# Performance work log

Hardware: AMD Instinct MI355X
Metric: run time of the kernel (lower is better)

## Reference

```python
import jax, jax.numpy as jnp
import numpy as np

B, C, H, W = 2, 512, 64, 64
S = 2            # scale_factor
HEADS = 8
GROUPS = 32      # assumed GroupNorm groups for group_norm(in_channels)
DK = C // HEADS
SCALE = 1.0 / DK ** 2   # faithful to source: 1/d_k**2
RES = H // S
R = RES * 2 - 1


def setup_inputs() -> dict:
    key = jax.random.key(0)
    ks = jax.random.split(key, 8)
    f = lambda k, shp, s=0.02: jax.random.normal(k, shp, jnp.float32) * s
    return {
        "x": jax.random.normal(ks[0], (B, C, H, W), jnp.float32),
        "q_w": f(ks[1], (C, C, 1, 1)),
        "q_b": jnp.zeros((C,), jnp.float32),
        "kv_w": f(ks[2], (2 * C, C, 1, 1)),
        "kv_b": jnp.zeros((2 * C,), jnp.float32),
        "off1_w": f(ks[3], (C, C, S, S)),
        "off1_b": jnp.zeros((C,), jnp.float32),
        "gn_w": jnp.ones((C,), jnp.float32),
        "gn_b": jnp.zeros((C,), jnp.float32),
        "off2_w": f(ks[4], (2, C, 1, 1)),
        "rpe_table": f(ks[5], (HEADS, R, R), 0.01),
        "proj_w": f(ks[6], (C, C, 1, 1)),
        "proj_b": jnp.zeros((C,), jnp.float32),
    }


def _conv(x, w, b=None, stride=1):
    y = jax.lax.conv_general_dilated(x, w, (stride, stride), 'VALID',
                                     dimension_numbers=('NCHW', 'OIHW', 'NCHW'))
    return y if b is None else y + b[None, :, None, None]


def _group_norm(x, w, b, eps=1e-5):
    n, c, h, wd = x.shape
    xg = x.reshape(n, GROUPS, -1)
    mu = xg.mean(-1, keepdims=True)
    var = xg.var(-1, keepdims=True)
    xg = (xg - mu) * jax.lax.rsqrt(var + eps)
    return xg.reshape(n, c, h, wd) * w[None, :, None, None] + b[None, :, None, None]


def _grid_sample(img, grid):
    # bilinear, align_corners=True; img [B,C,H,W], grid [B,...,2] in (x,y) order
    Bn, Cn, Hn, Wn = img.shape
    gshape = grid.shape[1:-1]
    g = grid.reshape(Bn, -1, 2)
    x = (g[..., 0] + 1.0) * 0.5 * (Wn - 1)
    y = (g[..., 1] + 1.0) * 0.5 * (Hn - 1)
    x0 = jnp.floor(x); y0 = jnp.floor(y)
    wx = (x - x0)[:, None, :]; wy = (y - y0)[:, None, :]
    x0i = jnp.clip(x0.astype(jnp.int32), 0, Wn - 1)
    x1i = jnp.clip(x0i + 1, 0, Wn - 1)
    y0i = jnp.clip(y0.astype(jnp.int32), 0, Hn - 1)
    y1i = jnp.clip(y0i + 1, 0, Hn - 1)
    imf = img.reshape(Bn, Cn, Hn * Wn)
    gat = lambda yi, xi: jnp.take_along_axis(imf, (yi * Wn + xi)[:, None, :], axis=2)
    out = (gat(y0i, x0i) * (1 - wx) * (1 - wy) + gat(y0i, x1i) * wx * (1 - wy)
           + gat(y1i, x0i) * (1 - wx) * wy + gat(y1i, x1i) * wx * wy)
    return out.reshape(Bn, Cn, *gshape)


def _forward(x, q_w, q_b, kv_w, kv_b, off1_w, off1_b, gn_w, gn_b, off2_w,
             rpe_table, proj_w, proj_b):
    l = H * W
    q = _conv(x, q_w, q_b)                                   # [B,C,H,W]
    t = _conv(q, off1_w, off1_b, stride=S)                   # [B,C,h,w]
    t = jax.nn.gelu(_group_norm(t, gn_w, gn_b), approximate=False)
    offset = _conv(t, off2_w).transpose(0, 2, 3, 1)          # [B,h,w,2] (y,x)
    h, w = offset.shape[1], offset.shape[2]
    n = h * w
    # reference points (linspace 0.5..h-0.5, normalized by h-1)
    ry = (jnp.linspace(0.5, h - 0.5, h) / (h - 1.0)) * 2.0 - 1.0
    rx = (jnp.linspace(0.5, w - 0.5, w) / (w - 1.0)) * 2.0 - 1.0
    ref = jnp.stack(jnp.meshgrid(ry, rx, indexing='ij'), -1)  # [h,w,2]
    pos = jnp.clip(offset + ref[None], -1.0, 1.0)             # [B,h,w,2]
    sampled = _grid_sample(x, pos[..., ::-1])                 # [B,C,h,w] (context=x)
    kv = _conv(sampled.reshape(B, C, 1, n), kv_w, kv_b)       # [B,2C,1,n]
    k, v = kv[:, :C], kv[:, C:]
    qf = q.reshape(B * HEADS, DK, l)
    kf = k.reshape(B * HEADS, DK, n)
    vf = v.reshape(B * HEADS, DK, n)
    attn = jnp.einsum('bcm,bcn->bmn', qf, kf) * SCALE         # [B*H, l, n]
    # query grid (arange, normalized by dim-1)
    gy = jnp.arange(H, dtype=jnp.float32) / (H - 1.0) * 2.0 - 1.0
    gx = jnp.arange(W, dtype=jnp.float32) / (W - 1.0) * 2.0 - 1.0
    qg = jnp.stack(jnp.meshgrid(gy, gx, indexing='ij'), -1).reshape(l, 2)
    disp = (qg[None, :, None, :] - pos.reshape(B, 1, n, 2)) * 0.5  # [B,l,n,2]
    rpe = jnp.broadcast_to(rpe_table[None], (B, HEADS, R, R))
    bias = _grid_sample(rpe, disp[..., ::-1])                  # [B,HEADS,l,n]
    attn = jax.nn.softmax(attn + bias.reshape(B * HEADS, l, n), axis=-1)
    out = jnp.einsum('bmn,bcn->bcm', attn, vf).reshape(B, C, H, W)
    return _conv(out, proj_w, proj_b)


def reference(x, q_w, q_b, kv_w, kv_b, off1_w, off1_b, gn_w, gn_b, off2_w,
              rpe_table, proj_w, proj_b):
    return _forward(x, q_w, q_b, kv_w, kv_b, off1_w, off1_b, gn_w, gn_b,
                    off2_w, rpe_table, proj_w, proj_b)
```

## Files before the change

kernel.cpp:

```cpp
#include <hip/hip_runtime.h>
#include <hip/hip_bf16.h>
#include <math.h>

typedef float floatx4 __attribute__((ext_vector_type(4)));
typedef short shortx8 __attribute__((ext_vector_type(8)));
typedef unsigned short ush;

#define NB    2
#define NC    512
#define NL    4096
#define NN    1024
#define NH    8
#define NDK   64
#define NR    63
#define LOG2E 1.44269504f
#define QT_SCALE (1.44269504f/4096.0f)

#define OFF_Q      0u
#define OFF_AO     0u
#define OFF_SMP    2097152u
#define OFF_QT     4194304u
#define OFF_T      6291456u
#define OFF_GS     7340032u
#define OFF_POS    7340160u
#define OFF_KT     7344256u
#define OFF_VV     7868544u
#define OFF_PART   8392832u
#define OFF_TAB2   8392832u

__device__ __forceinline__ ush f2bf(float f) {
    unsigned u = __float_as_uint(f);
    u += 0x7fffu + ((u >> 16) & 1u);
    return (ush)(u >> 16);
}
__device__ __forceinline__ float bf2f(ush h) {
    return __uint_as_float(((unsigned)h) << 16);
}

template<int NP, int BSRC, int OUTMODE>
__global__ __launch_bounds__(256) void gemm_mfma_k(
    const float* __restrict__ A, const void* __restrict__ Bv,
    const float* __restrict__ bias, void* __restrict__ Yv, void* __restrict__ Y2,
    int M, int K, int P, int KS)
{
    __shared__ ush a_hi[128 * 72];
    __shared__ ush b_hi[64 * 72];
    __shared__ ush a_lo[NP == 3 ? 128 * 72 : 64];
    __shared__ ush b_lo[NP == 3 ? 64 * 72 : 64];

    int tid = threadIdx.x;
    int wv = tid >> 6, lane = tid & 63, quad = lane >> 4, l15 = lane & 15;
    int bz = blockIdx.z;
    int b = bz / KS, ks = bz - b * KS;
    int m0 = blockIdx.y * 128, p0 = blockIdx.x * 64;
    int Ksl = K / KS, kbeg = ks * Ksl;

    floatx4 acc[2][4];
    #pragma unroll
    for (int mt = 0; mt < 2; ++mt)
        #pragma unroll
        for (int pt = 0; pt < 4; ++pt) acc[mt][pt] = (floatx4)0.f;

    for (int kc = 0; kc < Ksl; kc += 64) {
        int kg0 = kbeg + kc;
        #pragma unroll
        for (int r = 0; r < 8; ++r) {
            int idx = r * 256 + tid;
            int m = idx >> 4, k4 = (idx & 15) << 2;
            float4 av = *(const float4*)(A + (size_t)(m0 + m) * K + kg0 + k4);
            int o = m * 72 + k4;
            ush h0 = f2bf(av.x), h1 = f2bf(av.y), h2 = f2bf(av.z), h3 = f2bf(av.w);
            a_hi[o] = h0; a_hi[o + 1] = h1; a_hi[o + 2] = h2; a_hi[o + 3] = h3;
            if (NP == 3) {
                a_lo[o]     = f2bf(av.x - bf2f(h0));
                a_lo[o + 1] = f2bf(av.y - bf2f(h1));
                a_lo[o + 2] = f2bf(av.z - bf2f(h2));
                a_lo[o + 3] = f2bf(av.w - bf2f(h3));
            }
        }
        #pragma unroll
        for (int r = 0; r < 8; ++r) {
            int idx = r * 256 + tid;
            int k = idx >> 5, p2 = (idx & 31) << 1;
            float v0, v1;
            if (BSRC == 0) {
                const float* Bp = (const float*)Bv + (size_t)b * K * P;
                float2 t2 = *(const float2*)(Bp + (size_t)(kg0 + k) * P + p0 + p2);
                v0 = t2.x; v1 = t2.y;
            } else if (BSRC == 1) {
                const float* Bp = (const float*)Bv + (size_t)b * NC * NL;
                int kk = kg0 + k;
                int c = kk >> 2, kh = (kk >> 1) & 1, kw = kk & 1;
                int p = p0 + p2;
                int oh = p >> 5, ow = p & 31;
                const float* base = Bp + (size_t)c * NL + (2 * oh + kh) * 64 + kw;
                v0 = base[2 * ow];
                v1 = base[2 * ow + 2];
            } else {
                const ush* Bp = (const ush*)Bv + (size_t)b * K * P;
                unsigned u = *(const unsigned*)(Bp + (size_t)(kg0 + k) * P + p0 + p2);
                v0 = bf2f((ush)(u & 0xffffu));
                v1 = bf2f((ush)(u >> 16));
            }
            ush h0 = f2bf(v0), h1 = f2bf(v1);
            b_hi[p2 * 72 + k] = h0;
            b_hi[(p2 + 1) * 72 + k] = h1;
            if (NP == 3) {
                b_lo[p2 * 72 + k]       = f2bf(v0 - bf2f(h0));
                b_lo[(p2 + 1) * 72 + k] = f2bf(v1 - bf2f(h1));
            }
        }
        __syncthreads();

        shortx8 ah[2][2], al[2][2];
        #pragma unroll
        for (int mt = 0; mt < 2; ++mt)
            #pragma unroll
            for (int kk = 0; kk < 2; ++kk) {
                int o = (wv * 32 + mt * 16 + l15) * 72 + kk * 32 + quad * 8;
                ah[mt][kk] = *(const shortx8*)&a_hi[o];
                if (NP == 3) al[mt][kk] = *(const shortx8*)&a_lo[o];
            }
        #pragma unroll
        for (int pt = 0; pt < 4; ++pt) {
            #pragma unroll
            for (int kk = 0; kk < 2; ++kk) {
                int o = (pt * 16 + l15) * 72 + kk * 32 + quad * 8;
                shortx8 bh = *(const shortx8*)&b_hi[o];
                acc[0][pt] = __builtin_amdgcn_mfma_f32_16x16x32_bf16(ah[0][kk], bh, acc[0][pt], 0, 0, 0);
                acc[1][pt] = __builtin_amdgcn_mfma_f32_16x16x32_bf16(ah[1][kk], bh, acc[1][pt], 0, 0, 0);
                if (NP == 3) {
                    shortx8 bl = *(const shortx8*)&b_lo[o];
                    acc[0][pt] = __builtin_amdgcn_mfma_f32_16x16x32_bf16(ah[0][kk], bl, acc[0][pt], 0, 0, 0);
                    acc[1][pt] = __builtin_amdgcn_mfma_f32_16x16x32_bf16(ah[1][kk], bl, acc[1][pt], 0, 0, 0);
                    acc[0][pt] = __builtin_amdgcn_mfma_f32_16x16x32_bf16(al[0][kk], bh, acc[0][pt], 0, 0, 0);
                    acc[1][pt] = __builtin_amdgcn_mfma_f32_16x16x32_bf16(al[1][kk], bh, acc[1][pt], 0, 0, 0);
                }
            }
        }
        __syncthreads();
    }

    #pragma unroll
    for (int mt = 0; mt < 2; ++mt) {
        #pragma unroll
        for (int reg = 0; reg < 4; ++reg) {
            int m = m0 + wv * 32 + mt * 16 + quad * 4 + reg;
            float bb = (OUTMODE == 2) ? 0.f : bias[m];
            #pragma unroll
            for (int pt = 0; pt < 4; ++pt) {
                int p = p0 + pt * 16 + l15;
                float val = acc[mt][pt][reg] + bb;
                if (OUTMODE == 0) {
                    ((float*)Yv)[(size_t)b * M * P + (size_t)m * P + p] = val;
                } else if (OUTMODE == 2) {
                    ((float*)Yv)[(size_t)(ks * NB + b) * M * P + (size_t)m * P + p] = val;
                } else if (OUTMODE == 3) {
                    ((float*)Yv)[(size_t)b * M * P + (size_t)m * P + p] = val;
                    int h = m >> 6, d = m & 63;
                    ((ush*)Y2)[(((size_t)(b * 8 + h) * 4096) + p) * 64 + d] = f2bf(val * QT_SCALE);
                } else {
                    if (m < 512) {
                        int h = m >> 6, d = m & 63;
                        ((ush*)Yv)[(((size_t)(b * 8 + h) * 1024) + p) * 64 + d] = f2bf(val);
                    } else {
                        int c = m - 512;
                        ((ush*)Y2)[((size_t)(b * 512) + c) * 1024 + p] = f2bf(val);
                    }
                }
            }
        }
    }
}

__global__ __launch_bounds__(256) void reduce_off1_k(const float* __restrict__ part,
                                                     const float* __restrict__ bias,
                                                     float* __restrict__ t)
{
    int i = blockIdx.x * 256 + threadIdx.x;
    float v = part[i] + part[i + 1048576] + part[i + 2097152] + part[i + 3145728];
    t[i] = v + bias[(i >> 10) & 511];
}

__global__ __launch_bounds__(256) void gn_stats_k(const float* __restrict__ T, float* __restrict__ gs)
{
    int bg = blockIdx.x;
    const float* base = T + (size_t)bg * 16384;
    float s = 0.f, ss = 0.f;
    for (int i = threadIdx.x; i < 16384; i += 256) { float v = base[i]; s += v; ss += v * v; }
    #pragma unroll
    for (int off = 32; off >= 1; off >>= 1) { s += __shfl_xor(s, off); ss += __shfl_xor(ss, off); }
    __shared__ float red[8];
    int wv = threadIdx.x >> 6;
    if ((threadIdx.x & 63) == 0) { red[wv * 2] = s; red[wv * 2 + 1] = ss; }
    __syncthreads();
    if (threadIdx.x == 0) {
        float S = red[0] + red[2] + red[4] + red[6];
        float SS = red[1] + red[3] + red[5] + red[7];
        float mu = S / 16384.f;
        float var = SS / 16384.f - mu * mu;
        gs[bg * 2] = mu;
        gs[bg * 2 + 1] = rsqrtf(var + 1e-5f);
    }
}

__global__ __launch_bounds__(256) void gn_gelu_k(float* __restrict__ T, const float* __restrict__ gs,
                                                 const float* __restrict__ gw, const float* __restrict__ gb)
{
    int idx = blockIdx.x * 256 + threadIdx.x;
    int bg = idx >> 14;
    int c = (idx >> 10) & 511;
    float mu = gs[bg * 2], rs = gs[bg * 2 + 1];
    float v = (T[idx] - mu) * rs * gw[c] + gb[c];
    T[idx] = v * 0.5f * (1.f + erff(v * 0.70710678118654752f));
}

__global__ __launch_bounds__(256) void offset_pos_k(const float* __restrict__ T,
                                                    const float* __restrict__ w2,
                                                    float* __restrict__ pos)
{
    int b = blockIdx.x >> 5;
    int og = threadIdx.x & 31;
    int cg = threadIdx.x >> 5;
    int op = ((blockIdx.x & 31) << 5) + og;
    const float* Tb = T + (size_t)b * NC * NN + (size_t)cg * 64 * NN + op;
    float o0 = 0.f, o1 = 0.f;
    #pragma unroll 4
    for (int c = 0; c < 64; ++c) {
        float tv = Tb[(size_t)c * NN];
        o0 += w2[cg * 64 + c] * tv;
        o1 += w2[512 + cg * 64 + c] * tv;
    }
    __shared__ float rs[2][8][32];
    rs[0][cg][og] = o0;
    rs[1][cg][og] = o1;
    __syncthreads();
    if (threadIdx.x < 64) {
        int coord = threadIdx.x >> 5, og2 = threadIdx.x & 31;
        float s = 0.f;
        #pragma unroll
        for (int k = 0; k < 8; ++k) s += rs[coord][k][og2];
        int opf = ((blockIdx.x & 31) << 5) + og2;
        int oh = opf >> 5, ow = opf & 31;
        float ref = (coord == 0) ? ((0.5f + oh) / 31.f * 2.f - 1.f)
                                 : ((0.5f + ow) / 31.f * 2.f - 1.f);
        pos[((size_t)b * 1024 + opf) * 2 + coord] = fminf(fmaxf(s + ref, -1.f), 1.f);
    }
}

__global__ __launch_bounds__(256) void sample_k(const float* __restrict__ x,
                                                const float* __restrict__ pos,
                                                ush* __restrict__ smp)
{
    int idx = blockIdx.x * 256 + threadIdx.x;
    int j = idx & 1023, c = (idx >> 10) & 511, b = idx >> 19;
    float py = pos[(b * 1024 + j) * 2];
    float px = pos[(b * 1024 + j) * 2 + 1];
    float fx = (px + 1.f) * 0.5f * 63.f;
    float fy = (py + 1.f) * 0.5f * 63.f;
    float flx = floorf(fx), fly = floorf(fy);
    float wx = fx - flx, wy = fy - fly;
    int x0 = min(max((int)flx, 0), 63), y0 = min(max((int)fly, 0), 63);
    int x1 = min(x0 + 1, 63),           y1 = min(y0 + 1, 63);
    const float* xb = x + ((size_t)(b * NC + c)) * NL;
    float v00 = xb[y0 * 64 + x0];
    float v01 = xb[y0 * 64 + x1];
    float v10 = xb[y1 * 64 + x0];
    float v11 = xb[y1 * 64 + x1];
    float v = v00 * (1 - wx) * (1 - wy) + v01 * wx * (1 - wy)
            + v10 * (1 - wx) * wy       + v11 * wx * wy;
    smp[idx] = f2bf(v);
}

__global__ __launch_bounds__(256) void tab2_k(const float* __restrict__ rpe,
                                              unsigned* __restrict__ tab2)
{
    int i = blockIdx.x * 256 + threadIdx.x;
    int h = i >> 12, y = (i >> 6) & 63, x = i & 63;
    const float* R = rpe + (size_t)h * 3969;
    float v0 = (y < 63 && x < 63)     ? R[y * 63 + x] * LOG2E : 0.f;
    float v1 = (y < 63 && x + 1 < 63) ? R[y * 63 + x + 1] * LOG2E : 0.f;
    tab2[i] = (unsigned)f2bf(v0) | ((unsigned)f2bf(v1) << 16);
}

__global__ __launch_bounds__(256) void attn_k(
    const ush* __restrict__ qT, const ush* __restrict__ kT,
    const ush* __restrict__ vv, const float* __restrict__ pos,
    const unsigned* __restrict__ tab2, ush* __restrict__ ao)
{
    __shared__ __align__(16) char smem[33792];
    ush*      pa     = (ush*)smem;
    unsigned* tab_s  = (unsigned*)(smem + 9216);
    float*    posj15 = (float*)(smem + 25600);
    float*    obuf   = (float*)smem;

    int bh = blockIdx.y;
    int b = bh >> 3, h = bh & 7;
    int m0 = blockIdx.x * 64;
    int tid = threadIdx.x;
    int wv = tid >> 6, lane = tid & 63, quad = lane >> 4, l15 = lane & 15;

    const ush* qbase = qT + ((size_t)bh * 4096 + m0 + wv * 16 + l15) * 64 + quad * 8;
    shortx8 qf0 = *(const shortx8*)(qbase);
    shortx8 qf1 = *(const shortx8*)(qbase + 32);

    const uint2* tg = (const uint2*)(tab2 + (size_t)h * 4096);
    uint2* tab_s2 = (uint2*)tab_s;
    for (int i = tid; i < 2048; i += 256) tab_s2[i] = tg[i];
    const float* pb = pos + (size_t)b * 2048;
    for (int i = tid; i < 2048; i += 256) posj15[i] = pb[i] * 15.5f;

    float qy15[4], qx15[4];
    #pragma unroll
    for (int reg = 0; reg < 4; ++reg) {
        int mg = m0 + wv * 16 + quad * 4 + reg;
        qy15[reg] = (float)(mg >> 6) * (31.f / 63.f) + 15.5f;
        qx15[reg] = (float)(mg & 63) * (31.f / 63.f) + 15.5f;
    }

    floatx4 o_acc[4], o_sum;
    #pragma unroll
    for (int dt = 0; dt < 4; ++dt) o_acc[dt] = (floatx4)0.f;
    o_sum = (floatx4)0.f;
    shortx8 vone = {16256, 16256, 16256, 16256, 16256, 16256, 16256, 16256};

    __syncthreads();

    const ush* kbase = kT + (size_t)bh * 1024 * 64;
    const ush* vbase = vv + (size_t)(b * 512 + h * 64) * 1024;

    for (int jc = 0; jc < 16; ++jc) {
        int j0 = jc * 64;
        floatx4 sacc[4];
        #pragma unroll
        for (int jt = 0; jt < 4; ++jt) sacc[jt] = (floatx4)0.f;
        #pragma unroll
        for (int jt = 0; jt < 4; ++jt) {
            const ush* kp = kbase + (size_t)(j0 + jt * 16 + l15) * 64 + quad * 8;
            shortx8 kf0 = *(const shortx8*)kp;
            shortx8 kf1 = *(const shortx8*)(kp + 32);
            sacc[jt] = __builtin_amdgcn_mfma_f32_16x16x32_bf16(qf0, kf0, sacc[jt], 0, 0, 0);
            sacc[jt] = __builtin_amdgcn_mfma_f32_16x16x32_bf16(qf1, kf1, sacc[jt], 0, 0, 0);
        }
        #pragma unroll
        for (int jt = 0; jt < 4; ++jt) {
            int j = j0 + jt * 16 + l15;
            float2 pp = *(const float2*)&posj15[j * 2];
            #pragma unroll
            for (int reg = 0; reg < 4; ++reg) {
                float gy = qy15[reg] - pp.x;
                float gx = qx15[reg] - pp.y;
                float fy = floorf(gy), fx = floorf(gx);
                float wy = gy - fy, wx = gx - fx;
                int y0 = min(max((int)fy, 0), 62);
                int x0 = min(max((int)fx, 0), 62);
                unsigned tw0 = tab_s[(y0 << 6) + x0];
                unsigned tw1 = tab_s[(y0 << 6) + 64 + x0];
                float r00 = __uint_as_float(tw0 << 16);
                float r01 = __uint_as_float(tw0 & 0xffff0000u);
                float r10 = __uint_as_float(tw1 << 16);
                float r11 = __uint_as_float(tw1 & 0xffff0000u);
                float bx0 = r00 + wx * (r01 - r00);
                float bx1 = r10 + wx * (r11 - r10);
                float p = exp2f(sacc[jt][reg] + (bx0 + wy * (bx1 - bx0)));
                pa[(wv * 16 + quad * 4 + reg) * 72 + jt * 16 + l15] = f2bf(p);
            }
        }
        const ush* pbase = pa + (wv * 16 + l15) * 72 + quad * 8;
        shortx8 pf0 = *(const shortx8*)pbase;
        shortx8 pf1 = *(const shortx8*)(pbase + 32);
        o_sum = __builtin_amdgcn_mfma_f32_16x16x32_bf16(pf0, vone, o_sum, 0, 0, 0);
        o_sum = __builtin_amdgcn_mfma_f32_16x16x32_bf16(pf1, vone, o_sum, 0, 0, 0);
        #pragma unroll
        for (int dt = 0; dt < 4; ++dt) {
            const ush* vp = vbase + (size_t)(dt * 16 + l15) * 1024 + j0 + quad * 8;
            shortx8 vf0 = *(const shortx8*)vp;
            shortx8 vf1 = *(const shortx8*)(vp + 32);
            o_acc[dt] = __builtin_amdgcn_mfma_f32_16x16x32_bf16(pf0, vf0, o_acc[dt], 0, 0, 0);
            o_acc[dt] = __builtin_amdgcn_mfma_f32_16x16x32_bf16(pf1, vf1, o_acc[dt], 0, 0, 0);
        }
    }

    __syncthreads();
    float inv[4];
    #pragma unroll
    for (int reg = 0; reg < 4; ++reg) inv[reg] = 1.f / o_sum[reg];
    #pragma unroll
    for (int dt = 0; dt < 4; ++dt)
        #pragma unroll
        for (int reg = 0; reg < 4; ++reg)
            obuf[(dt * 16 + l15) * 68 + wv * 16 + quad * 4 + reg] = o_acc[dt][reg] * inv[reg];
    __syncthreads();
    ush* aobase = ao + ((size_t)(b * 512 + h * 64)) * 4096 + m0;
    for (int i = tid; i < 4096; i += 256) {
        int d = i >> 6, m = i & 63;
        aobase[(size_t)d * 4096 + m] = f2bf(obuf[d * 68 + m]);
    }
}

extern "C" void kernel_launch(void* const* d_in, const int* in_sizes, int n_in,
                              void* d_out, int out_size, void* d_ws, size_t ws_size,
                              hipStream_t stream) {
    const float* x      = (const float*)d_in[0];
    const float* q_w    = (const float*)d_in[1];
    const float* q_b    = (const float*)d_in[2];
    const float* kv_w   = (const float*)d_in[3];
    const float* kv_b   = (const float*)d_in[4];
    const float* off1_w = (const float*)d_in[5];
    const float* off1_b = (const float*)d_in[6];
    const float* gn_w   = (const float*)d_in[7];
    const float* gn_b   = (const float*)d_in[8];
    const float* off2_w = (const float*)d_in[9];
    const float* rpe    = (const float*)d_in[10];
    const float* proj_w = (const float*)d_in[11];
    const float* proj_b = (const float*)d_in[12];

    float* ws   = (float*)d_ws;
    float* q    = ws + OFF_Q;
    ush*   ao   = (ush*)(ws + OFF_AO);
    ush*   smp  = (ush*)(ws + OFF_SMP);
    ush*   qT   = (ush*)(ws + OFF_QT);
    float* t    = ws + OFF_T;
    float* gs   = ws + OFF_GS;
    float* pos  = ws + OFF_POS;
    ush*   kT   = (ush*)(ws + OFF_KT);
    ush*   vv   = (ush*)(ws + OFF_VV);
    float* part = ws + OFF_PART;
    unsigned* tab2 = (unsigned*)(ws + OFF_TAB2);
    float* out  = (float*)d_out;

    gemm_mfma_k<3, 0, 3><<<dim3(64, 4, 2), 256, 0, stream>>>(q_w, x, q_b, q, qT, 512, 512, 4096, 1);
    gemm_mfma_k<3, 1, 2><<<dim3(16, 4, 8), 256, 0, stream>>>(off1_w, q, nullptr, part, nullptr, 512, 2048, 1024, 4);
    reduce_off1_k<<<4096, 256, 0, stream>>>(part, off1_b, t);
    gn_stats_k<<<64, 256, 0, stream>>>(t, gs);
    gn_gelu_k<<<4096, 256, 0, stream>>>(t, gs, gn_w, gn_b);
    offset_pos_k<<<64, 256, 0, stream>>>(t, off2_w, pos);
    tab2_k<<<128, 256, 0, stream>>>(rpe, tab2);
    sample_k<<<4096, 256, 0, stream>>>(x, pos, smp);
    gemm_mfma_k<1, 2, 4><<<dim3(16, 8, 2), 256, 0, stream>>>(kv_w, smp, kv_b, kT, vv, 1024, 512, 1024, 1);
    attn_k<<<dim3(64, 16), 256, 0, stream>>>(qT, kT, vv, pos, tab2, ao);
    gemm_mfma_k<1, 2, 0><<<dim3(64, 4, 2), 256, 0, stream>>>(proj_w, ao, proj_b, out, nullptr, 512, 512, 4096, 1);
}
```

Before: 361.8 us.

## Vectorize GEMM B-tile loads, swizzle RPE table, prefetch V, simplify bilinear indexing

Measured after the change: 394.5 us. 9.0% more time.

```diff
diff --git a/kernel.cpp b/kernel.cpp
--- a/kernel.cpp
+++ b/kernel.cpp
@@ -5,6 +5,7 @@
 typedef float floatx4 __attribute__((ext_vector_type(4)));
 typedef short shortx8 __attribute__((ext_vector_type(8)));
 typedef unsigned short ush;
+typedef ush ushx4 __attribute__((ext_vector_type(4)));
 
 #define NB    2
 #define NC    512
@@ -79,35 +80,51 @@
             }
         }
         #pragma unroll
-        for (int r = 0; r < 8; ++r) {
-            int idx = r * 256 + tid;
-            int k = idx >> 5, p2 = (idx & 31) << 1;
-            float v0, v1;
-            if (BSRC == 0) {
+        for (int r = 0; r < 4; ++r) {
+            int e = r * 256 + tid;
+            if (BSRC == 1) {
+                int k2 = e >> 5;
+                int p2 = (e & 31) << 1;
+                int kk = kg0 + (k2 << 1);
+                int c = kk >> 2, kh = (kk >> 1) & 1;
+                int p = p0 + p2, oh = p >> 5, ow = p & 31;
+                const float* Bp = (const float*)Bv + (size_t)b * NC * NL;
+                float4 av = *(const float4*)(Bp + (size_t)c * NL + (2 * oh + kh) * 64 + 2 * ow);
+                int kl = k2 << 1;
+                ush h0 = f2bf(av.x), h1 = f2bf(av.y), h2 = f2bf(av.z), h3 = f2bf(av.w);
+                b_hi[p2 * 72 + kl]           = h0;
+                b_hi[p2 * 72 + kl + 1]       = h1;
+                b_hi[(p2 + 1) * 72 + kl]     = h2;
+                b_hi[(p2 + 1) * 72 + kl + 1] = h3;
+                if (NP == 3) {
+                    b_lo[p2 * 72 + kl]           = f2bf(av.x - bf2f(h0));
+                    b_lo[p2 * 72 + kl + 1]       = f2bf(av.y - bf2f(h1));
+                    b_lo[(p2 + 1) * 72 + kl]     = f2bf(av.z - bf2f(h2));
+                    b_lo[(p2 + 1) * 72 + kl + 1] = f2bf(av.w - bf2f(h3));
+                }
+            } else if (BSRC == 0) {
+                int k = e >> 4, p4 = (e & 15) << 2;
                 const float* Bp = (const float*)Bv + (size_t)b * K * P;
-                float2 t2 = *(const float2*)(Bp + (size_t)(kg0 + k) * P + p0 + p2);
-                v0 = t2.x; v1 = t2.y;
-            } else if (BSRC == 1) {
-                const float* Bp = (const float*)Bv + (size_t)b * NC * NL;
-                int kk = kg0 + k;
-                int c = kk >> 2, kh = (kk >> 1) & 1, kw = kk & 1;
-                int p = p0 + p2;
-                int oh = p >> 5, ow = p & 31;
-                const float* base = Bp + (size_t)c * NL + (2 * oh + kh) * 64 + kw;
-                v0 = base[2 * ow];
-                v1 = base[2 * ow + 2];
+                float4 av = *(const float4*)(Bp + (size_t)(kg0 + k) * P + p0 + p4);
+                ush h0 = f2bf(av.x), h1 = f2bf(av.y), h2 = f2bf(av.z), h3 = f2bf(av.w);
+                b_hi[p4 * 72 + k]       = h0;
+                b_hi[(p4 + 1) * 72 + k] = h1;
+                b_hi[(p4 + 2) * 72 + k] = h2;
+                b_hi[(p4 + 3) * 72 + k] = h3;
+                if (NP == 3) {
+                    b_lo[p4 * 72 + k]       = f2bf(av.x - bf2f(h0));
+                    b_lo[(p4 + 1) * 72 + k] = f2bf(av.y - bf2f(h1));
+                    b_lo[(p4 + 2) * 72 + k] = f2bf(av.z - bf2f(h2));
+                    b_lo[(p4 + 3) * 72 + k] = f2bf(av.w - bf2f(h3));
+                }
             } else {
+                int k = e >> 4, p4 = (e & 15) << 2;
                 const ush* Bp = (const ush*)Bv + (size_t)b * K * P;
-                unsigned u = *(const unsigned*)(Bp + (size_t)(kg0 + k) * P + p0 + p2);
-                v0 = bf2f((ush)(u & 0xffffu));
-                v1 = bf2f((ush)(u >> 16));
-            }
-            ush h0 = f2bf(v0), h1 = f2bf(v1);
-            b_hi[p2 * 72 + k] = h0;
-            b_hi[(p2 + 1) * 72 + k] = h1;
-            if (NP == 3) {
-                b_lo[p2 * 72 + k]       = f2bf(v0 - bf2f(h0));
-                b_lo[(p2 + 1) * 72 + k] = f2bf(v1 - bf2f(h1));
+                ushx4 uv = *(const ushx4*)(Bp + (size_t)(kg0 + k) * P + p0 + p4);
+                b_hi[p4 * 72 + k]       = uv.x;
+                b_hi[(p4 + 1) * 72 + k] = uv.y;
+                b_hi[(p4 + 2) * 72 + k] = uv.z;
+                b_hi[(p4 + 3) * 72 + k] = uv.w;
             }
         }
         __syncthreads();
@@ -280,7 +297,8 @@
     const float* R = rpe + (size_t)h * 3969;
     float v0 = (y < 63 && x < 63)     ? R[y * 63 + x] * LOG2E : 0.f;
     float v1 = (y < 63 && x + 1 < 63) ? R[y * 63 + x + 1] * LOG2E : 0.f;
-    tab2[i] = (unsigned)f2bf(v0) | ((unsigned)f2bf(v1) << 16);
+    int xs = x ^ (y & 31);
+    tab2[(h << 12) + (y << 6) + xs] = (unsigned)f2bf(v0) | ((unsigned)f2bf(v1) << 16);
 }
 
 __global__ __launch_bounds__(256) void attn_k(
@@ -341,6 +359,13 @@
             shortx8 kf1 = *(const shortx8*)(kp + 32);
             sacc[jt] = __builtin_amdgcn_mfma_f32_16x16x32_bf16(qf0, kf0, sacc[jt], 0, 0, 0);
             sacc[jt] = __builtin_amdgcn_mfma_f32_16x16x32_bf16(qf1, kf1, sacc[jt], 0, 0, 0);
+        }
+        shortx8 vf[4][2];
+        #pragma unroll
+        for (int dt = 0; dt < 4; ++dt) {
+            const ush* vp = vbase + (size_t)(dt * 16 + l15) * 1024 + j0 + quad * 8;
+            vf[dt][0] = *(const shortx8*)vp;
+            vf[dt][1] = *(const shortx8*)(vp + 32);
         }
         #pragma unroll
         for (int jt = 0; jt < 4; ++jt) {
@@ -350,12 +375,13 @@
             for (int reg = 0; reg < 4; ++reg) {
                 float gy = qy15[reg] - pp.x;
                 float gx = qx15[reg] - pp.y;
-                float fy = floorf(gy), fx = floorf(gx);
-                float wy = gy - fy, wx = gx - fx;
-                int y0 = min(max((int)fy, 0), 62);
-                int x0 = min(max((int)fx, 0), 62);
-                unsigned tw0 = tab_s[(y0 << 6) + x0];
-                unsigned tw1 = tab_s[(y0 << 6) + 64 + x0];
+                int y0 = (int)gy;
+                int x0 = (int)gx;
+                float wy = gy - (float)y0;
+                float wx = gx - (float)x0;
+                int y1 = y0 + 1;
+                unsigned tw0 = tab_s[(y0 << 6) + (x0 ^ (y0 & 31))];
+                unsigned tw1 = tab_s[(y1 << 6) + (x0 ^ (y1 & 31))];
                 float r00 = __uint_as_float(tw0 << 16);
                 float r01 = __uint_as_float(tw0 & 0xffff0000u);
                 float r10 = __uint_as_float(tw1 << 16);
@@ -373,11 +399,8 @@
         o_sum = __builtin_amdgcn_mfma_f32_16x16x32_bf16(pf1, vone, o_sum, 0, 0, 0);
         #pragma unroll
         for (int dt = 0; dt < 4; ++dt) {
-            const ush* vp = vbase + (size_t)(dt * 16 + l15) * 1024 + j0 + quad * 8;
-            shortx8 vf0 = *(const shortx8*)vp;
-            shortx8 vf1 = *(const shortx8*)(vp + 32);
-            o_acc[dt] = __builtin_amdgcn_mfma_f32_16x16x32_bf16(pf0, vf0, o_acc[dt], 0, 0, 0);
-            o_acc[dt] = __builtin_amdgcn_mfma_f32_16x16x32_bf16(pf1, vf1, o_acc[dt], 0, 0, 0);
+            o_acc[dt] = __builtin_amdgcn_mfma_f32_16x16x32_bf16(pf0, vf[dt][0], o_acc[dt], 0, 0, 0);
+            o_acc[dt] = __builtin_amdgcn_mfma_f32_16x16x32_bf16(pf1, vf[dt][1], o_acc[dt], 0, 0, 0);
         }
     }
 
```
